# Kernel optimization log

Hardware: AMD Instinct MI355X
Metric: run time of the kernel (lower is better)

## Reference

```python
import jax, jax.numpy as jnp
import numpy as np

MODES = 4
WIDTH = 8
IN_CH = 3
OUT_CH = 6
LAMBDA_RES = 0.3


def spectral_conv3d(x, w1, w2, w3, w4):
    # x: [B, C, D, H, W] real. Standard FNO3d SpectralConv3d:
    # rfftn over last 3 dims, multiply low modes in 4 corner octants, irfftn.
    B, C, D, H, W = x.shape
    m = MODES
    x_ft = jnp.fft.rfftn(x, axes=(-3, -2, -1))  # [B,C,D,H,W//2+1] complex

    def mul(blk, w):
        return jnp.einsum('bixyz,ioxyz->boxyz', blk, w)

    out_ft = jnp.zeros((B, w1.shape[1], D, H, W // 2 + 1), dtype=x_ft.dtype)
    out_ft = out_ft.at[:, :, :m, :m, :m].set(mul(x_ft[:, :, :m, :m, :m], w1))
    out_ft = out_ft.at[:, :, -m:, :m, :m].set(mul(x_ft[:, :, -m:, :m, :m], w2))
    out_ft = out_ft.at[:, :, :m, -m:, :m].set(mul(x_ft[:, :, :m, -m:, :m], w3))
    out_ft = out_ft.at[:, :, -m:, -m:, :m].set(mul(x_ft[:, :, -m:, -m:, :m], w4))
    return jnp.fft.irfftn(out_ft, s=(D, H, W), axes=(-3, -2, -1))


def fno3d(u, fc0_w, fc0_b, spec_ws, conv_ws, conv_bs, fc1_w, fc1_b, fc2_w, fc2_b):
    # Lift: 1x1 conv via einsum (channels-first)
    x = jnp.einsum('bcdhw,oc->bodhw', u, fc0_w) + fc0_b[None, :, None, None, None]
    for i in range(4):
        w1, w2, w3, w4 = spec_ws[i]
        x1 = spectral_conv3d(x, w1, w2, w3, w4)
        x2 = jnp.einsum('bcdhw,oc->bodhw', x, conv_ws[i]) + conv_bs[i][None, :, None, None, None]
        x = x1 + x2
        if i < 3:
            x = jax.nn.gelu(x)
    x = jnp.einsum('bcdhw,oc->bodhw', x, fc1_w) + fc1_b[None, :, None, None, None]
    x = jax.nn.gelu(x)
    x = jnp.einsum('bcdhw,oc->bodhw', x, fc2_w) + fc2_b[None, :, None, None, None]
    return x


def setup_inputs() -> dict:
    key = jax.random.key(0)
    ks = jax.random.split(key, 32)
    B, D, H, W = 8, 64, 64, 64
    m, wd = MODES, WIDTH
    u = jax.random.normal(ks[0], (B, IN_CH, D, H, W), dtype=jnp.float32)
    scale = 1.0 / (wd * wd)
    spec_ws = []
    ki = 1
    for _ in range(4):
        layer = []
        for _ in range(4):
            re = jax.random.uniform(ks[ki], (wd, wd, m, m, m)) * scale
            im = jax.random.uniform(ks[ki + 1], (wd, wd, m, m, m)) * scale
            layer.append(re + 1j * im)
            ki += 2
        spec_ws.append(tuple(layer))
    conv_ws = [jax.random.normal(ks[ki + i], (wd, wd)) * (1.0 / wd) for i in range(4)]
    ki += 4
    conv_bs = [jnp.zeros((wd,), jnp.float32) for _ in range(4)]
    fc0_w = jax.random.normal(ks[ki], (wd, IN_CH)) * 0.3; ki += 1
    fc0_b = jnp.zeros((wd,), jnp.float32)
    fc1_w = jax.random.normal(ks[ki], (4 * wd, wd)) * 0.2; ki += 1
    fc1_b = jnp.zeros((4 * wd,), jnp.float32)
    fc2_w = jax.random.normal(ks[ki], (OUT_CH, 4 * wd)) * 0.2; ki += 1
    fc2_b = jnp.zeros((OUT_CH,), jnp.float32)
    nu = jnp.asarray(0.001, jnp.float32)
    return {
        'u': u, 'nu': nu,
        'fc0_w': fc0_w, 'fc0_b': fc0_b,
        'spec_ws': spec_ws, 'conv_ws': conv_ws, 'conv_bs': conv_bs,
        'fc1_w': fc1_w, 'fc1_b': fc1_b, 'fc2_w': fc2_w, 'fc2_b': fc2_b,
    }


def reference(u, nu, fc0_w, fc0_b, spec_ws, conv_ws, conv_bs, fc1_w, fc1_b, fc2_w, fc2_b):
    B, C, D, H, W = u.shape
    # hard core: zeros [B,6,D,H,W] with first 3 channels = u*nu
    hard = jnp.concatenate([u * nu, jnp.zeros((B, 3, D, H, W), u.dtype)], axis=1)
    soft = fno3d(u, fc0_w, fc0_b, spec_ws, conv_ws, conv_bs, fc1_w, fc1_b, fc2_w, fc2_b)
    return hard + LAMBDA_RES * soft
```

## Files before the change

### kernel.cpp

```cpp
#include <hip/hip_runtime.h>


#define TWO_PI_OVER_64 0.09817477042468103

__device__ __forceinline__ float gelu_fast(float x) {
    float x2 = x * x;
    float p  = x * (1.0f + 0.044715f * x2);
    float e  = __builtin_amdgcn_exp2f(-2.3022083f * p);
    return x * __builtin_amdgcn_rcpf(1.0f + e);
}

#define BUILD_TW() \
    __shared__ float twc[64], tws[64]; \
    if (threadIdx.x < 64) { \
        double a_ = TWO_PI_OVER_64 * (double)threadIdx.x; \
        twc[threadIdx.x] = (float)cos(a_); tws[threadIdx.x] = (float)sin(a_); \
    }

#define ROR_STEP(x, CTRL) \
    x += __int_as_float(__builtin_amdgcn_update_dpp( \
            0, __float_as_int(x), CTRL, 0xF, 0xF, true))

__device__ __forceinline__ float red16_ror(float x) {
    ROR_STEP(x, 0x121);
    ROR_STEP(x, 0x122);
    ROR_STEP(x, 0x124);
    ROR_STEP(x, 0x128);
    return x;
}

__device__ __forceinline__ void a_tail_store(
    const float v[4], const float c1[4], const float s1[4],
    const float c2[4], const float s2[4], const float c3[4], const float s3[4],
    int wq, float2* __restrict__ Arow)
{
    float p0  = v[0] + v[1] + v[2] + v[3];
    float ar1 = v[0]*c1[0] + v[1]*c1[1] + v[2]*c1[2] + v[3]*c1[3];
    float ai1 = -(v[0]*s1[0] + v[1]*s1[1] + v[2]*s1[2] + v[3]*s1[3]);
    float ar2 = v[0]*c2[0] + v[1]*c2[1] + v[2]*c2[2] + v[3]*c2[3];
    float ai2 = -(v[0]*s2[0] + v[1]*s2[1] + v[2]*s2[2] + v[3]*s2[3]);
    float ar3 = v[0]*c3[0] + v[1]*c3[1] + v[2]*c3[2] + v[3]*c3[3];
    float ai3 = -(v[0]*s3[0] + v[1]*s3[1] + v[2]*s3[2] + v[3]*s3[3]);
    p0  = red16_ror(p0);
    ar1 = red16_ror(ar1);  ai1 = red16_ror(ai1);
    ar2 = red16_ror(ar2);  ai2 = red16_ror(ai2);
    ar3 = red16_ror(ar3);  ai3 = red16_ror(ai3);
    if (wq < 2) {
        float4 av;
        av.x = (wq == 0) ? p0   : ar2;
        av.y = (wq == 0) ? 0.f  : ai2;
        av.z = (wq == 0) ? ar1  : ar3;
        av.w = (wq == 0) ? ai1  : ai3;
        *((float4*)Arow + wq) = av;
    }
}

__global__ __launch_bounds__(256) void k_liftA(
    const float* __restrict__ u, const float* __restrict__ fc0w,
    const float* __restrict__ fc0b, float* __restrict__ x,
    float2* __restrict__ A)
{
    BUILD_TW();
    const int t = threadIdx.x, bid = blockIdx.x;
    const int b = bid >> 8, dx = (bid >> 2) & 63, dy0 = (bid & 3) * 16;
    const int dyl = t >> 4, wq = t & 15;
    const size_t sp = (size_t)dx * 4096 + (size_t)(dy0 + dyl) * 64 + wq * 4;
    float uin[3][4];
    #pragma unroll
    for (int c = 0; c < 3; ++c) {
        float4 v = *(const float4*)&u[(size_t)(b * 3 + c) * 262144 + sp];
        uin[c][0] = v.x; uin[c][1] = v.y; uin[c][2] = v.z; uin[c][3] = v.w;
    }
    __syncthreads();
    float c1[4], s1[4], c2[4], s2[4], c3[4], s3[4];
    #pragma unroll
    for (int j = 0; j < 4; ++j) {
        int w = wq * 4 + j;
        c1[j] = twc[w];             s1[j] = tws[w];
        c2[j] = twc[(2 * w) & 63];  s2[j] = tws[(2 * w) & 63];
        c3[j] = twc[(3 * w) & 63];  s3[j] = tws[(3 * w) & 63];
    }
    #pragma unroll
    for (int o = 0; o < 8; ++o) {
        float w0 = fc0w[o * 3 + 0], w1 = fc0w[o * 3 + 1], w2 = fc0w[o * 3 + 2];
        float bb = fc0b[o];
        float v[4];
        #pragma unroll
        for (int j = 0; j < 4; ++j)
            v[j] = bb + uin[0][j] * w0 + uin[1][j] * w1 + uin[2][j] * w2;
        *(float4*)&x[(size_t)(b * 8 + o) * 262144 + sp] =
            make_float4(v[0], v[1], v[2], v[3]);
        a_tail_store(v, c1, s1, c2, s2, c3, s3, wq,
                     A + ((size_t)(b * 8 + o) * 4096 + dx * 64 + dy0 + dyl) * 4);
    }
}

__global__ __launch_bounds__(256) void k_fH(const float2* __restrict__ A,
                                            float2* __restrict__ Bh)
{
    BUILD_TW();
    __syncthreads();
    const int g = blockIdx.x * 256 + threadIdx.x;
    const int triple = g >> 5, idx = g & 31;
    const int ky = idx >> 2, kz = idx & 3;
    const int b = triple >> 9, c = (triple >> 6) & 7, dx = triple & 63;
    const int kyv = ky < 4 ? ky : ky + 56;
    const float2* Ap = A + (size_t)(b * 8 + c) * 16384 + dx * 256 + kz;
    float re = 0.f, im = 0.f;
    int ti = 0;
    #pragma unroll 8
    for (int dy = 0; dy < 64; ++dy) {
        float2 a = Ap[dy * 4];
        float cc = twc[ti], ss = tws[ti];
        re += a.x * cc + a.y * ss;
        im += a.y * cc - a.x * ss;
        ti = (ti + kyv) & 63;
    }
    Bh[(size_t)(b * 8 + c) * 2048 + dx * 32 + ky * 4 + kz] = make_float2(re, im);
}

__global__ __launch_bounds__(256) void k_fDmix(
    const float2* __restrict__ Bh,
    const float2* __restrict__ w1, const float2* __restrict__ w2,
    const float2* __restrict__ w3, const float2* __restrict__ w4,
    float2* __restrict__ O)
{
    BUILD_TW();
    __shared__ float2 Cs[256];
    const int t = threadIdx.x, bid = blockIdx.x;
    const int b = bid >> 3, kx = bid & 7;
    const int kxv = kx < 4 ? kx : kx + 56;
    __syncthreads();
    {
        int kz = t & 3, ky = (t >> 2) & 7, c = t >> 5;
        const float2* Bp = Bh + (size_t)(b * 8 + c) * 2048 + ky * 4 + kz;
        float re = 0.f, im = 0.f;
        int ti = 0;
        #pragma unroll 8
        for (int dx = 0; dx < 64; ++dx) {
            float2 v = Bp[dx * 32];
            float cc = twc[ti], ss = tws[ti];
            re += v.x * cc + v.y * ss;
            im += v.y * cc - v.x * ss;
            ti = (ti + kxv) & 63;
        }
        Cs[t] = make_float2(re, im);
    }
    __syncthreads();
    {
        int kz = t & 3, ky = (t >> 2) & 7, o = t >> 5;
        const float2* wsel = (kx < 4) ? ((ky < 4) ? w1 : w3) : ((ky < 4) ? w2 : w4);
        int kxw = kx & 3, kyw = ky & 3;
        float re = 0.f, im = 0.f;
        #pragma unroll
        for (int i = 0; i < 8; ++i) {
            float2 cv = Cs[i * 32 + ky * 4 + kz];
            float2 wv = wsel[(((size_t)(i * 8 + o) * 4 + kxw) * 4 + kyw) * 4 + kz];
            re += cv.x * wv.x - cv.y * wv.y;
            im += cv.x * wv.y + cv.y * wv.x;
        }
        O[(((size_t)(b * 8 + o) * 8 + kx) * 8 + ky) * 4 + kz] = make_float2(re, im);
    }
}

__global__ __launch_bounds__(256, 4) void k_ptA(
    float* __restrict__ x, const float2* __restrict__ O,
    const float* __restrict__ cw, const float* __restrict__ cb,
    float2* __restrict__ A)
{
    BUILD_TW();
    __shared__ float2 Ps[256];
    __shared__ float2 Qs[8 * 16 * 4];
    const int t = threadIdx.x, bid = blockIdx.x;
    const int b = bid >> 8, dx = (bid >> 2) & 63, dy0 = (bid & 3) * 16;
    const int dyl = t >> 4, wq = t & 15;
    const size_t sp = (size_t)dx * 4096 + (size_t)(dy0 + dyl) * 64 + wq * 4;
    float4 xv[8];
    #pragma unroll
    for (int c = 0; c < 8; ++c)
        xv[c] = *(const float4*)&x[(size_t)(b * 8 + c) * 262144 + sp];
    const int pkz = t & 3, pky = (t >> 2) & 7, po = t >> 5;
    float2 ov[8];
    #pragma unroll
    for (int kxi = 0; kxi < 8; ++kxi)
        ov[kxi] = O[(((size_t)(b * 8 + po) * 8 + kxi) * 8 + pky) * 4 + pkz];
    __syncthreads();
    {
        float re = 0.f, im = 0.f;
        #pragma unroll
        for (int kxi = 0; kxi < 8; ++kxi) {
            int kxv = kxi < 4 ? kxi : kxi + 56;
            int ti = (kxv * dx) & 63;
            float cc = twc[ti], ss = tws[ti];
            re += ov[kxi].x * cc - ov[kxi].y * ss;
            im += ov[kxi].y * cc + ov[kxi].x * ss;
        }
        Ps[t] = make_float2(re, im);
    }
    __syncthreads();
    for (int it = t; it < 512; it += 256) {
        int kz = it & 3, qdyl = (it >> 2) & 15, o = it >> 6;
        int dy = dy0 + qdyl;
        float re = 0.f, im = 0.f;
        #pragma unroll
        for (int kyi = 0; kyi < 8; ++kyi) {
            int kyv = kyi < 4 ? kyi : kyi + 56;
            int ti = (kyv * dy) & 63;
            float2 v = Ps[(o * 8 + kyi) * 4 + kz];
            float cc = twc[ti], ss = tws[ti];
            re += v.x * cc - v.y * ss;
            im += v.y * cc + v.x * ss;
        }
        Qs[(o * 16 + qdyl) * 4 + kz] = make_float2(re, im);
    }
    __syncthreads();
    float c1[4], s1[4], c2[4], s2[4], c3[4], s3[4];
    #pragma unroll
    for (int j = 0; j < 4; ++j) {
        int w = wq * 4 + j;
        c1[j] = twc[w];             s1[j] = tws[w];
        c2[j] = twc[(2 * w) & 63];  s2[j] = tws[(2 * w) & 63];
        c3[j] = twc[(3 * w) & 63];  s3[j] = tws[(3 * w) & 63];
    }
    const float invN3 = 1.0f / 262144.0f;
    #pragma unroll
    for (int o = 0; o < 8; ++o) {
        float4 qa = *(const float4*)&Qs[(o * 16 + dyl) * 4];
        float4 qb = *(const float4*)&Qs[(o * 16 + dyl) * 4 + 2];
        float outj[4];
        #pragma unroll
        for (int j = 0; j < 4; ++j) {
            float x1 = qa.x + 2.f * (qa.z * c1[j] - qa.w * s1[j]
                                   + qb.x * c2[j] - qb.y * s2[j]
                                   + qb.z * c3[j] - qb.w * s3[j]);
            x1 *= invN3;
            float x2 = cb[o];
            #pragma unroll
            for (int c = 0; c < 8; ++c) {
                const float* xc = &xv[c].x;
                x2 += cw[o * 8 + c] * xc[j];
            }
            outj[j] = gelu_fast(x1 + x2);
        }
        *(float4*)&x[(size_t)(b * 8 + o) * 262144 + sp] =
            make_float4(outj[0], outj[1], outj[2], outj[3]);
        a_tail_store(outj, c1, s1, c2, s2, c3, s3, wq,
                     A + ((size_t)(b * 8 + o) * 4096 + dx * 64 + dy0 + dyl) * 4);
    }
}

__global__ __launch_bounds__(256, 4) void k_ptout(
    const float* __restrict__ x, const float2* __restrict__ O,
    const float* __restrict__ cw, const float* __restrict__ cb,
    const float* __restrict__ u, const float* __restrict__ nu,
    const float* __restrict__ fc1w, const float* __restrict__ fc1b,
    const float* __restrict__ fc2w, const float* __restrict__ fc2b,
    float* __restrict__ out)
{
    BUILD_TW();
    __shared__ float2 Ps[256];
    __shared__ float2 Qs[8 * 16 * 4];
    const int t = threadIdx.x, bid = blockIdx.x;
    const int b = bid >> 8, dx = (bid >> 2) & 63, dy0 = (bid & 3) * 16;
    const int dyl = t >> 4, wq = t & 15;
    const size_t sp = (size_t)dx * 4096 + (size_t)(dy0 + dyl) * 64 + wq * 4;
    float4 xv[8];
    #pragma unroll
    for (int c = 0; c < 8; ++c)
        xv[c] = *(const float4*)&x[(size_t)(b * 8 + c) * 262144 + sp];
    float4 uv[3];
    #pragma unroll
    for (int c = 0; c < 3; ++c)
        uv[c] = *(const float4*)&u[(size_t)(b * 3 + c) * 262144 + sp];
    const int pkz = t & 3, pky = (t >> 2) & 7, po = t >> 5;
    float2 ovv[8];
    #pragma unroll
    for (int kxi = 0; kxi < 8; ++kxi)
        ovv[kxi] = O[(((size_t)(b * 8 + po) * 8 + kxi) * 8 + pky) * 4 + pkz];
    __syncthreads();
    {
        float re = 0.f, im = 0.f;
        #pragma unroll
        for (int kxi = 0; kxi < 8; ++kxi) {
            int kxv = kxi < 4 ? kxi : kxi + 56;
            int ti = (kxv * dx) & 63;
            float cc = twc[ti], ss = tws[ti];
            re += ovv[kxi].x * cc - ovv[kxi].y * ss;
            im += ovv[kxi].y * cc + ovv[kxi].x * ss;
        }
        Ps[t] = make_float2(re, im);
    }
    __syncthreads();
    for (int it = t; it < 512; it += 256) {
        int kz = it & 3, qdyl = (it >> 2) & 15, o = it >> 6;
        int dy = dy0 + qdyl;
        float re = 0.f, im = 0.f;
        #pragma unroll
        for (int kyi = 0; kyi < 8; ++kyi) {
            int kyv = kyi < 4 ? kyi : kyi + 56;
            int ti = (kyv * dy) & 63;
            float2 v = Ps[(o * 8 + kyi) * 4 + kz];
            float cc = twc[ti], ss = tws[ti];
            re += v.x * cc - v.y * ss;
            im += v.y * cc + v.x * ss;
        }
        Qs[(o * 16 + qdyl) * 4 + kz] = make_float2(re, im);
    }
    __syncthreads();
    float c1[4], s1[4], c2[4], s2[4], c3[4], s3[4];
    #pragma unroll
    for (int j = 0; j < 4; ++j) {
        int w = wq * 4 + j;
        c1[j] = twc[w];             s1[j] = tws[w];
        c2[j] = twc[(2 * w) & 63];  s2[j] = tws[(2 * w) & 63];
        c3[j] = twc[(3 * w) & 63];  s3[j] = tws[(3 * w) & 63];
    }
    const float invN3 = 1.0f / 262144.0f;
    float vv[8][4];
    #pragma unroll
    for (int o = 0; o < 8; ++o) {
        float4 qa = *(const float4*)&Qs[(o * 16 + dyl) * 4];
        float4 qb = *(const float4*)&Qs[(o * 16 + dyl) * 4 + 2];
        #pragma unroll
        for (int j = 0; j < 4; ++j) {
            float x1 = qa.x + 2.f * (qa.z * c1[j] - qa.w * s1[j]
                                   + qb.x * c2[j] - qb.y * s2[j]
                                   + qb.z * c3[j] - qb.w * s3[j]);
            x1 *= invN3;
            float x2 = cb[o];
            #pragma unroll
            for (int c = 0; c < 8; ++c) {
                const float* xc = &xv[c].x;
                x2 += cw[o * 8 + c] * xc[j];
            }
            vv[o][j] = x1 + x2;
        }
    }
    float so[6][4];
    #pragma unroll
    for (int c6 = 0; c6 < 6; ++c6)
        #pragma unroll
        for (int j = 0; j < 4; ++j) so[c6][j] = fc2b[c6];
    #pragma unroll 4
    for (int h = 0; h < 32; ++h) {
        float wr[8];
        #pragma unroll
        for (int c = 0; c < 8; ++c) wr[c] = fc1w[h * 8 + c];
        const float hb = fc1b[h];
        float w2r[6];
        #pragma unroll
        for (int c6 = 0; c6 < 6; ++c6) w2r[c6] = fc2w[c6 * 32 + h];
        #pragma unroll
        for (int j = 0; j < 4; ++j) {
            float a = hb;
            #pragma unroll
            for (int c = 0; c < 8; ++c) a += vv[c][j] * wr[c];
            float g = gelu_fast(a);
            #pragma unroll
            for (int c6 = 0; c6 < 6; ++c6) so[c6][j] += g * w2r[c6];
        }
    }
    const float nuv = nu[0];
    #pragma unroll
    for (int c6 = 0; c6 < 6; ++c6) {
        float4 res;
        float* rp = &res.x;
        if (c6 < 3) {
            const float* up = &uv[c6].x;
            #pragma unroll
            for (int j = 0; j < 4; ++j) rp[j] = 0.3f * so[c6][j] + up[j] * nuv;
        } else {
            #pragma unroll
            for (int j = 0; j < 4; ++j) rp[j] = 0.3f * so[c6][j];
        }
        *(float4*)&out[(size_t)(b * 6 + c6) * 262144 + sp] = res;
    }
}

struct PackPtrs { const float* re[16]; const float* im[16]; };

__global__ __launch_bounds__(256) void k_pack_all(PackPtrs p, float2* __restrict__ dst)
{
    int i = blockIdx.x * 256 + threadIdx.x;
    int w = i >> 12, idx = i & 4095;
    dst[i] = make_float2(p.re[w][idx], p.im[w][idx]);
}

extern "C" void kernel_launch(void* const* d_in, const int* in_sizes, int n_in,
                              void* d_out, int out_size, void* d_ws, size_t ws_size,
                              hipStream_t stream)
{
    (void)out_size;
    const char* leaf[32];
    bool spec_split = false;
    const char* spec_re[16]; const char* spec_im[16];
    int src = 0;
    leaf[0] = (const char*)d_in[src++];
    leaf[1] = (const char*)d_in[src++];
    leaf[2] = (const char*)d_in[src++];
    leaf[3] = (const char*)d_in[src++];
    {
        int s = (src < n_in) ? in_sizes[src] : 4096;
        if (n_in >= 48 && s == 4096) {
            spec_split = true;
            for (int i = 0; i < 16; ++i) {
                spec_re[i] = (const char*)d_in[src++];
                spec_im[i] = (const char*)d_in[src++];
            }
        } else {
            int per;
            if (s == 4096 || s == 8192) per = 1;
            else if (s == 16384 || s == 32768) per = 4;
            else per = 16;
            for (int i = 0; i < 16; i += per) {
                const char* base = (const char*)d_in[src++];
                for (int j = 0; j < per; ++j) leaf[4 + i + j] = base + (size_t)j * 4096 * 8;
            }
        }
    }
    {
        int s = (src < n_in) ? in_sizes[src] : 64;
        if (s == 64) { for (int i = 0; i < 4; ++i) leaf[20 + i] = (const char*)d_in[src++]; }
        else { const char* base = (const char*)d_in[src++];
               for (int i = 0; i < 4; ++i) leaf[20 + i] = base + (size_t)i * 64 * 4; }
    }
    {
        int s = (src < n_in) ? in_sizes[src] : 8;
        if (s == 8) { for (int i = 0; i < 4; ++i) leaf[24 + i] = (const char*)d_in[src++]; }
        else { const char* base = (const char*)d_in[src++];
               for (int i = 0; i < 4; ++i) leaf[24 + i] = base + (size_t)i * 8 * 4; }
    }
    leaf[28] = (const char*)d_in[src++];
    leaf[29] = (const char*)d_in[src++];
    leaf[30] = (const char*)d_in[src++];
    leaf[31] = (const char*)d_in[src++];

    const float* u    = (const float*)leaf[0];
    const float* nu   = (const float*)leaf[1];
    const float* fc0w = (const float*)leaf[2];
    const float* fc0b = (const float*)leaf[3];
    const float* convw[4], *convb[4];
    for (int i = 0; i < 4; ++i) { convw[i] = (const float*)leaf[20 + i];
                                  convb[i] = (const float*)leaf[24 + i]; }
    const float* fc1w = (const float*)leaf[28];
    const float* fc1b = (const float*)leaf[29];
    const float* fc2w = (const float*)leaf[30];
    const float* fc2b = (const float*)leaf[31];

    const size_t szX = 67108864, szA = 8388608, szB = 1048576,
                 szO = 131072, szSP = 524288;
    char* ws = (char*)d_ws;
    float* xbuf = (float*)ws;
    float2 *Abuf, *Bbuf, *Obuf, *SP;
    if (ws_size >= szX + szA + szB + szO + szSP) {
        Abuf = (float2*)(ws + szX);
        Bbuf = (float2*)(ws + szX + szA);
        Obuf = (float2*)(ws + szX + szA + szB);
        SP   = (float2*)(ws + szX + szA + szB + szO);
    } else {
        Obuf = (float2*)(ws + szX);
        Abuf = (float2*)d_out;
        Bbuf = (float2*)((char*)d_out + szA);
        SP   = (float2*)((char*)d_out + szA + szB);
    }

    const float2* specw[16];
    if (spec_split) {
        PackPtrs pp;
        for (int i = 0; i < 16; ++i) {
            pp.re[i] = (const float*)spec_re[i];
            pp.im[i] = (const float*)spec_im[i];
            specw[i] = SP + (size_t)i * 4096;
        }
        hipLaunchKernelGGL(k_pack_all, dim3(256), dim3(256), 0, stream, pp, SP);
    } else {
        for (int i = 0; i < 16; ++i) specw[i] = (const float2*)leaf[4 + i];
    }
    float* outp = (float*)d_out;

    hipLaunchKernelGGL(k_liftA, dim3(2048), dim3(256), 0, stream, u, fc0w, fc0b, xbuf, Abuf);
    for (int L = 0; L < 4; ++L) {
        hipLaunchKernelGGL(k_fH, dim3(512), dim3(256), 0, stream, Abuf, Bbuf);
        hipLaunchKernelGGL(k_fDmix, dim3(64), dim3(256), 0, stream,
                           Bbuf, specw[L*4+0], specw[L*4+1], specw[L*4+2], specw[L*4+3], Obuf);
        if (L < 3) {
            hipLaunchKernelGGL(k_ptA, dim3(2048), dim3(256), 0, stream,
                               xbuf, Obuf, convw[L], convb[L], Abuf);
        } else {
            hipLaunchKernelGGL(k_ptout, dim3(2048), dim3(256), 0, stream,
                               xbuf, Obuf, convw[3], convb[3], u, nu,
                               fc1w, fc1b, fc2w, fc2b, outp);
        }
    }
}
```

Measured before the change: 288.2 us.

## Fuse ky-direction DFT into lift and pointwise kernels via LDS, drop k_fH

Each block in the lift and pointwise kernels now covers a whole dx plane (1024 threads over 64 dy rows) and keeps the per-row kz partial DFT in shared memory. The ky DFT is then done in-block with a 4-way split and DPP quad reduction, writing Bh directly. This removes the separate k_fH launch and the 8 MB A intermediate round trip through global memory. k_fDmix also splits its dx reduction across 4 lanes with 1024 threads. The cost is larger blocks, more shared memory and more barriers, which can reduce occupancy. The kernels also recompute the kx inverse DFT over all 64 dy rows per block.

```diff
diff --git a/kernel.cpp b/kernel.cpp
--- a/kernel.cpp
+++ b/kernel.cpp
@@ -29,10 +29,18 @@
     return x;
 }
 
-__device__ __forceinline__ void a_tail_store(
+__device__ __forceinline__ float red4_quad(float x) {
+    x += __int_as_float(__builtin_amdgcn_update_dpp(
+            0, __float_as_int(x), 0xB1, 0xF, 0xF, true));
+    x += __int_as_float(__builtin_amdgcn_update_dpp(
+            0, __float_as_int(x), 0x4E, 0xF, 0xF, true));
+    return x;
+}
+
+__device__ __forceinline__ void a_tail_lds(
     const float v[4], const float c1[4], const float s1[4],
     const float c2[4], const float s2[4], const float c3[4], const float s3[4],
-    int wq, float2* __restrict__ Arow)
+    int wq, float2* __restrict__ AsRow)
 {
     float p0  = v[0] + v[1] + v[2] + v[3];
     float ar1 = v[0]*c1[0] + v[1]*c1[1] + v[2]*c1[2] + v[3]*c1[3];
@@ -51,20 +59,48 @@
         av.y = (wq == 0) ? 0.f  : ai2;
         av.z = (wq == 0) ? ar1  : ar3;
         av.w = (wq == 0) ? ai1  : ai3;
-        *((float4*)Arow + wq) = av;
-    }
-}
-
-__global__ __launch_bounds__(256) void k_liftA(
+        *((float4*)AsRow + wq) = av;
+    }
+}
+
+__device__ __forceinline__ void ky_dft_store(
+    const float2* __restrict__ As, const float* __restrict__ twc,
+    const float* __restrict__ tws, int t, int b, int dx,
+    float2* __restrict__ Bh)
+{
+    const int out = t >> 2, q = t & 3;
+    const int c = out >> 5, ky = (out >> 2) & 7, kz = out & 3;
+    const int kyv = ky < 4 ? ky : ky + 56;
+    float re = 0.f, im = 0.f;
+    int ti = (kyv * q) & 63;
+    const int step = (kyv * 4) & 63;
+    #pragma unroll 4
+    for (int i = 0; i < 16; ++i) {
+        int dy = q + i * 4;
+        float2 a = As[(c * 64 + dy) * 4 + kz];
+        float cc = twc[ti], ss = tws[ti];
+        re += a.x * cc + a.y * ss;
+        im += a.y * cc - a.x * ss;
+        ti = (ti + step) & 63;
+    }
+    re = red4_quad(re);
+    im = red4_quad(im);
+    if (q == 0)
+        Bh[(size_t)(b * 8 + c) * 2048 + dx * 32 + ky * 4 + kz] =
+            make_float2(re, im);
+}
+
+__global__ __launch_bounds__(1024, 8) void k_liftA2(
     const float* __restrict__ u, const float* __restrict__ fc0w,
     const float* __restrict__ fc0b, float* __restrict__ x,
-    float2* __restrict__ A)
+    float2* __restrict__ Bh)
 {
     BUILD_TW();
+    __shared__ float2 As[8 * 64 * 4];
     const int t = threadIdx.x, bid = blockIdx.x;
-    const int b = bid >> 8, dx = (bid >> 2) & 63, dy0 = (bid & 3) * 16;
+    const int b = bid >> 6, dx = bid & 63;
     const int dyl = t >> 4, wq = t & 15;
-    const size_t sp = (size_t)dx * 4096 + (size_t)(dy0 + dyl) * 64 + wq * 4;
+    const size_t sp = (size_t)dx * 4096 + (size_t)dyl * 64 + wq * 4;
     float uin[3][4];
     #pragma unroll
     for (int c = 0; c < 3; ++c) {
@@ -90,36 +126,13 @@
             v[j] = bb + uin[0][j] * w0 + uin[1][j] * w1 + uin[2][j] * w2;
         *(float4*)&x[(size_t)(b * 8 + o) * 262144 + sp] =
             make_float4(v[0], v[1], v[2], v[3]);
-        a_tail_store(v, c1, s1, c2, s2, c3, s3, wq,
-                     A + ((size_t)(b * 8 + o) * 4096 + dx * 64 + dy0 + dyl) * 4);
-    }
-}
-
-__global__ __launch_bounds__(256) void k_fH(const float2* __restrict__ A,
-                                            float2* __restrict__ Bh)
-{
-    BUILD_TW();
-    __syncthreads();
-    const int g = blockIdx.x * 256 + threadIdx.x;
-    const int triple = g >> 5, idx = g & 31;
-    const int ky = idx >> 2, kz = idx & 3;
-    const int b = triple >> 9, c = (triple >> 6) & 7, dx = triple & 63;
-    const int kyv = ky < 4 ? ky : ky + 56;
-    const float2* Ap = A + (size_t)(b * 8 + c) * 16384 + dx * 256 + kz;
-    float re = 0.f, im = 0.f;
-    int ti = 0;
-    #pragma unroll 8
-    for (int dy = 0; dy < 64; ++dy) {
-        float2 a = Ap[dy * 4];
-        float cc = twc[ti], ss = tws[ti];
-        re += a.x * cc + a.y * ss;
-        im += a.y * cc - a.x * ss;
-        ti = (ti + kyv) & 63;
-    }
-    Bh[(size_t)(b * 8 + c) * 2048 + dx * 32 + ky * 4 + kz] = make_float2(re, im);
-}
-
-__global__ __launch_bounds__(256) void k_fDmix(
+        a_tail_lds(v, c1, s1, c2, s2, c3, s3, wq, &As[(o * 64 + dyl) * 4]);
+    }
+    __syncthreads();
+    ky_dft_store(As, twc, tws, t, b, dx, Bh);
+}
+
+__global__ __launch_bounds__(1024) void k_fDmix(
     const float2* __restrict__ Bh,
     const float2* __restrict__ w1, const float2* __restrict__ w2,
     const float2* __restrict__ w3, const float2* __restrict__ w4,
@@ -132,22 +145,26 @@
     const int kxv = kx < 4 ? kx : kx + 56;
     __syncthreads();
     {
-        int kz = t & 3, ky = (t >> 2) & 7, c = t >> 5;
+        const int out = t >> 2, q = t & 3;
+        const int kz = out & 3, ky = (out >> 2) & 7, c = out >> 5;
         const float2* Bp = Bh + (size_t)(b * 8 + c) * 2048 + ky * 4 + kz;
         float re = 0.f, im = 0.f;
-        int ti = 0;
-        #pragma unroll 8
-        for (int dx = 0; dx < 64; ++dx) {
-            float2 v = Bp[dx * 32];
+        int ti = (kxv * q) & 63;
+        const int step = (kxv * 4) & 63;
+        #pragma unroll 4
+        for (int i = 0; i < 16; ++i) {
+            float2 v = Bp[(q + i * 4) * 32];
             float cc = twc[ti], ss = tws[ti];
             re += v.x * cc + v.y * ss;
             im += v.y * cc - v.x * ss;
-            ti = (ti + kxv) & 63;
-        }
-        Cs[t] = make_float2(re, im);
-    }
-    __syncthreads();
-    {
+            ti = (ti + step) & 63;
+        }
+        re = red4_quad(re);
+        im = red4_quad(im);
+        if (q == 0) Cs[out] = make_float2(re, im);
+    }
+    __syncthreads();
+    if (t < 256) {
         int kz = t & 3, ky = (t >> 2) & 7, o = t >> 5;
         const float2* wsel = (kx < 4) ? ((ky < 4) ? w1 : w3) : ((ky < 4) ? w2 : w4);
         int kxw = kx & 3, kyw = ky & 3;
@@ -163,29 +180,32 @@
     }
 }
 
-__global__ __launch_bounds__(256, 4) void k_ptA(
+__global__ __launch_bounds__(1024, 8) void k_ptA2(
     float* __restrict__ x, const float2* __restrict__ O,
     const float* __restrict__ cw, const float* __restrict__ cb,
-    float2* __restrict__ A)
+    float2* __restrict__ Bh)
 {
     BUILD_TW();
     __shared__ float2 Ps[256];
-    __shared__ float2 Qs[8 * 16 * 4];
+    __shared__ float2 Qs[8 * 64 * 4];
+    __shared__ float2 As[8 * 64 * 4];
     const int t = threadIdx.x, bid = blockIdx.x;
-    const int b = bid >> 8, dx = (bid >> 2) & 63, dy0 = (bid & 3) * 16;
+    const int b = bid >> 6, dx = bid & 63;
     const int dyl = t >> 4, wq = t & 15;
-    const size_t sp = (size_t)dx * 4096 + (size_t)(dy0 + dyl) * 64 + wq * 4;
+    const size_t sp = (size_t)dx * 4096 + (size_t)dyl * 64 + wq * 4;
     float4 xv[8];
     #pragma unroll
     for (int c = 0; c < 8; ++c)
         xv[c] = *(const float4*)&x[(size_t)(b * 8 + c) * 262144 + sp];
-    const int pkz = t & 3, pky = (t >> 2) & 7, po = t >> 5;
     float2 ov[8];
-    #pragma unroll
-    for (int kxi = 0; kxi < 8; ++kxi)
-        ov[kxi] = O[(((size_t)(b * 8 + po) * 8 + kxi) * 8 + pky) * 4 + pkz];
-    __syncthreads();
-    {
+    if (t < 256) {
+        const int pkz = t & 3, pky = (t >> 2) & 7, po = t >> 5;
+        #pragma unroll
+        for (int kxi = 0; kxi < 8; ++kxi)
+            ov[kxi] = O[(((size_t)(b * 8 + po) * 8 + kxi) * 8 + pky) * 4 + pkz];
+    }
+    __syncthreads();
+    if (t < 256) {
         float re = 0.f, im = 0.f;
         #pragma unroll
         for (int kxi = 0; kxi < 8; ++kxi) {
@@ -198,9 +218,9 @@
         Ps[t] = make_float2(re, im);
     }
     __syncthreads();
-    for (int it = t; it < 512; it += 256) {
-        int kz = it & 3, qdyl = (it >> 2) & 15, o = it >> 6;
-        int dy = dy0 + qdyl;
+    #pragma unroll
+    for (int it = t; it < 2048; it += 1024) {
+        int kz = it & 3, dy = (it >> 2) & 63, o = it >> 8;
         float re = 0.f, im = 0.f;
         #pragma unroll
         for (int kyi = 0; kyi < 8; ++kyi) {
@@ -211,7 +231,7 @@
             re += v.x * cc - v.y * ss;
             im += v.y * cc + v.x * ss;
         }
-        Qs[(o * 16 + qdyl) * 4 + kz] = make_float2(re, im);
+        Qs[(o * 64 + dy) * 4 + kz] = make_float2(re, im);
     }
     __syncthreads();
     float c1[4], s1[4], c2[4], s2[4], c3[4], s3[4];
@@ -225,8 +245,8 @@
     const float invN3 = 1.0f / 262144.0f;
     #pragma unroll
     for (int o = 0; o < 8; ++o) {
-        float4 qa = *(const float4*)&Qs[(o * 16 + dyl) * 4];
-        float4 qb = *(const float4*)&Qs[(o * 16 + dyl) * 4 + 2];
+        float4 qa = *(const float4*)&Qs[(o * 64 + dyl) * 4];
+        float4 qb = *(const float4*)&Qs[(o * 64 + dyl) * 4 + 2];
         float outj[4];
         #pragma unroll
         for (int j = 0; j < 4; ++j) {
@@ -244,9 +264,10 @@
         }
         *(float4*)&x[(size_t)(b * 8 + o) * 262144 + sp] =
             make_float4(outj[0], outj[1], outj[2], outj[3]);
-        a_tail_store(outj, c1, s1, c2, s2, c3, s3, wq,
-                     A + ((size_t)(b * 8 + o) * 4096 + dx * 64 + dy0 + dyl) * 4);
-    }
+        a_tail_lds(outj, c1, s1, c2, s2, c3, s3, wq, &As[(o * 64 + dyl) * 4]);
+    }
+    __syncthreads();
+    ky_dft_store(As, twc, tws, t, b, dx, Bh);
 }
 
 __global__ __launch_bounds__(256, 4) void k_ptout(
@@ -447,21 +468,18 @@
     const float* fc2w = (const float*)leaf[30];
     const float* fc2b = (const float*)leaf[31];
 
-    const size_t szX = 67108864, szA = 8388608, szB = 1048576,
-                 szO = 131072, szSP = 524288;
+    const size_t szX = 67108864, szB = 1048576, szO = 131072, szSP = 524288;
     char* ws = (char*)d_ws;
     float* xbuf = (float*)ws;
-    float2 *Abuf, *Bbuf, *Obuf, *SP;
-    if (ws_size >= szX + szA + szB + szO + szSP) {
-        Abuf = (float2*)(ws + szX);
-        Bbuf = (float2*)(ws + szX + szA);
-        Obuf = (float2*)(ws + szX + szA + szB);
-        SP   = (float2*)(ws + szX + szA + szB + szO);
+    float2 *Bbuf, *Obuf, *SP;
+    if (ws_size >= szX + szB + szO + szSP) {
+        Bbuf = (float2*)(ws + szX);
+        Obuf = (float2*)(ws + szX + szB);
+        SP   = (float2*)(ws + szX + szB + szO);
     } else {
         Obuf = (float2*)(ws + szX);
-        Abuf = (float2*)d_out;
-        Bbuf = (float2*)((char*)d_out + szA);
-        SP   = (float2*)((char*)d_out + szA + szB);
+        Bbuf = (float2*)d_out;
+        SP   = (float2*)((char*)d_out + szB);
     }
 
     const float2* specw[16];
@@ -478,14 +496,14 @@
     }
     float* outp = (float*)d_out;
 
-    hipLaunchKernelGGL(k_liftA, dim3(2048), dim3(256), 0, stream, u, fc0w, fc0b, xbuf, Abuf);
+    hipLaunchKernelGGL(k_liftA2, dim3(512), dim3(1024), 0, stream,
+                       u, fc0w, fc0b, xbuf, Bbuf);
     for (int L = 0; L < 4; ++L) {
-        hipLaunchKernelGGL(k_fH, dim3(512), dim3(256), 0, stream, Abuf, Bbuf);
-        hipLaunchKernelGGL(k_fDmix, dim3(64), dim3(256), 0, stream,
+        hipLaunchKernelGGL(k_fDmix, dim3(64), dim3(1024), 0, stream,
                            Bbuf, specw[L*4+0], specw[L*4+1], specw[L*4+2], specw[L*4+3], Obuf);
         if (L < 3) {
-            hipLaunchKernelGGL(k_ptA, dim3(2048), dim3(256), 0, stream,
-                               xbuf, Obuf, convw[L], convb[L], Abuf);
+            hipLaunchKernelGGL(k_ptA2, dim3(512), dim3(1024), 0, stream,
+                               xbuf, Obuf, convw[L], convb[L], Bbuf);
         } else {
             hipLaunchKernelGGL(k_ptout, dim3(2048), dim3(256), 0, stream,
                                xbuf, Obuf, convw[3], convb[3], u, nu,
```

Result: slower. 716.1 us (+148.5%).

## Split DFT reductions across lane quads in k_fH and k_fDmix with DPP reduce

Applied to the files above, without the earlier changes.

Each output of the H-axis and D-axis partial DFTs is now computed by four lanes, each summing 16 of the 64 terms, and the partial sums are combined with quad DPP shuffles. k_fH also stages its 2048-element input slab in shared memory with coalesced float4 loads, replacing strided global reads. Both kernels move to 1024-thread blocks, which gives four times more threads for these small, latency-bound reductions. In exchange there is extra shuffle and shared-memory traffic, and three quarters of the lanes sit idle during stores and during the mixing phase of k_fDmix.

```diff
diff --git a/kernel.cpp b/kernel.cpp
--- a/kernel.cpp
+++ b/kernel.cpp
@@ -26,6 +26,14 @@
     ROR_STEP(x, 0x122);
     ROR_STEP(x, 0x124);
     ROR_STEP(x, 0x128);
+    return x;
+}
+
+__device__ __forceinline__ float red4_quad(float x) {
+    x += __int_as_float(__builtin_amdgcn_update_dpp(
+            0, __float_as_int(x), 0xB1, 0xF, 0xF, true));
+    x += __int_as_float(__builtin_amdgcn_update_dpp(
+            0, __float_as_int(x), 0x4E, 0xF, 0xF, true));
     return x;
 }
 
@@ -95,31 +103,39 @@
     }
 }
 
-__global__ __launch_bounds__(256) void k_fH(const float2* __restrict__ A,
-                                            float2* __restrict__ Bh)
+__global__ __launch_bounds__(1024, 4) void k_fH(const float2* __restrict__ A,
+                                                float2* __restrict__ Bh)
 {
     BUILD_TW();
-    __syncthreads();
-    const int g = blockIdx.x * 256 + threadIdx.x;
-    const int triple = g >> 5, idx = g & 31;
-    const int ky = idx >> 2, kz = idx & 3;
-    const int b = triple >> 9, c = (triple >> 6) & 7, dx = triple & 63;
+    __shared__ float2 As[2048];
+    const int t = threadIdx.x, bid = blockIdx.x;
+    const int b = bid >> 6, c = (bid >> 3) & 7, dxg = bid & 7;
+    const size_t base = (size_t)(b * 8 + c) * 16384 + (size_t)dxg * 2048;
+    ((float4*)As)[t] = ((const float4*)(A + base))[t];
+    __syncthreads();
+    const int out = t >> 2, q = t & 3;
+    const int kz = out & 3, ky = (out >> 2) & 7, dxl = out >> 5;
     const int kyv = ky < 4 ? ky : ky + 56;
-    const float2* Ap = A + (size_t)(b * 8 + c) * 16384 + dx * 256 + kz;
     float re = 0.f, im = 0.f;
-    int ti = 0;
-    #pragma unroll 8
-    for (int dy = 0; dy < 64; ++dy) {
-        float2 a = Ap[dy * 4];
+    int ti = (kyv * q) & 63;
+    const int step = (kyv * 4) & 63;
+    #pragma unroll 4
+    for (int i = 0; i < 16; ++i) {
+        int dy = q + i * 4;
+        float2 a = As[dxl * 256 + dy * 4 + kz];
         float cc = twc[ti], ss = tws[ti];
         re += a.x * cc + a.y * ss;
         im += a.y * cc - a.x * ss;
-        ti = (ti + kyv) & 63;
-    }
-    Bh[(size_t)(b * 8 + c) * 2048 + dx * 32 + ky * 4 + kz] = make_float2(re, im);
-}
-
-__global__ __launch_bounds__(256) void k_fDmix(
+        ti = (ti + step) & 63;
+    }
+    re = red4_quad(re);
+    im = red4_quad(im);
+    if (q == 0)
+        Bh[(size_t)(b * 8 + c) * 2048 + (dxg * 8 + dxl) * 32 + ky * 4 + kz] =
+            make_float2(re, im);
+}
+
+__global__ __launch_bounds__(1024) void k_fDmix(
     const float2* __restrict__ Bh,
     const float2* __restrict__ w1, const float2* __restrict__ w2,
     const float2* __restrict__ w3, const float2* __restrict__ w4,
@@ -132,22 +148,26 @@
     const int kxv = kx < 4 ? kx : kx + 56;
     __syncthreads();
     {
-        int kz = t & 3, ky = (t >> 2) & 7, c = t >> 5;
+        const int out = t >> 2, q = t & 3;
+        const int kz = out & 3, ky = (out >> 2) & 7, c = out >> 5;
         const float2* Bp = Bh + (size_t)(b * 8 + c) * 2048 + ky * 4 + kz;
         float re = 0.f, im = 0.f;
-        int ti = 0;
-        #pragma unroll 8
-        for (int dx = 0; dx < 64; ++dx) {
-            float2 v = Bp[dx * 32];
+        int ti = (kxv * q) & 63;
+        const int step = (kxv * 4) & 63;
+        #pragma unroll 4
+        for (int i = 0; i < 16; ++i) {
+            float2 v = Bp[(q + i * 4) * 32];
             float cc = twc[ti], ss = tws[ti];
             re += v.x * cc + v.y * ss;
             im += v.y * cc - v.x * ss;
-            ti = (ti + kxv) & 63;
-        }
-        Cs[t] = make_float2(re, im);
-    }
-    __syncthreads();
-    {
+            ti = (ti + step) & 63;
+        }
+        re = red4_quad(re);
+        im = red4_quad(im);
+        if (q == 0) Cs[out] = make_float2(re, im);
+    }
+    __syncthreads();
+    if (t < 256) {
         int kz = t & 3, ky = (t >> 2) & 7, o = t >> 5;
         const float2* wsel = (kx < 4) ? ((ky < 4) ? w1 : w3) : ((ky < 4) ? w2 : w4);
         int kxw = kx & 3, kyw = ky & 3;
@@ -480,8 +500,8 @@
 
     hipLaunchKernelGGL(k_liftA, dim3(2048), dim3(256), 0, stream, u, fc0w, fc0b, xbuf, Abuf);
     for (int L = 0; L < 4; ++L) {
-        hipLaunchKernelGGL(k_fH, dim3(512), dim3(256), 0, stream, Abuf, Bbuf);
-        hipLaunchKernelGGL(k_fDmix, dim3(64), dim3(256), 0, stream,
+        hipLaunchKernelGGL(k_fH, dim3(512), dim3(1024), 0, stream, Abuf, Bbuf);
+        hipLaunchKernelGGL(k_fDmix, dim3(64), dim3(1024), 0, stream,
                            Bbuf, specw[L*4+0], specw[L*4+1], specw[L*4+2], specw[L*4+3], Obuf);
         if (L < 3) {
             hipLaunchKernelGGL(k_ptA, dim3(2048), dim3(256), 0, stream,
```

Measured after the change: 294.8 us. 1.02x slower.
